# Performance work log

Measured on AMD Instinct MI355X. Metric: run time of the kernel, lower is better.

## Reference

```python
import jax, jax.numpy as jnp
import numpy as np

RADIUS = 2
B, C, D, H, W = 2, 16, 48, 128, 256
G = 3 * (2 * RADIUS + 1) ** 2  # 75 guidance channels: (2r+1)^2 spatial x 3 depth offsets


def setup_inputs() -> dict:
    key = jax.random.key(0)
    k1, k2 = jax.random.split(key)
    input1 = jax.random.normal(k1, (B, C, D, H, W), dtype=jnp.float32)  # cost volume
    input2 = jax.random.normal(k2, (B, G, H, W), dtype=jnp.float32) * 0.1  # guidance weights
    return {"input1": input1, "input2": input2}


def _lga3d(x, g, r):
    """One pass of local guided aggregation.
    x: [B,C,D,H,W] cost volume; g: [B, 3*(2r+1)^2, H, W] per-pixel weights.
    out[b,c,d,h,w] = sum_{i,j in (2r+1)^2 window, k in {d-1,d,d+1}}
                     g[b, (i*(2r+1)+j)*3+k, h, w] * x[b,c,d+k-1,h+i-r,w+j-r]
    (zero padding out of bounds; weights shared across channels)."""
    w = 2 * r + 1
    bb, cc, dd, hh, ww = x.shape
    # pad depth by 1 on each side, spatial by r on each side
    xp = jnp.pad(x, ((0, 0), (0, 0), (1, 1), (r, r), (r, r)))
    out = jnp.zeros_like(x)
    for i in range(w):          # fixed small window loop (not a data-dim loop)
        for j in range(w):
            for k in range(3):  # depth offsets -1, 0, +1
                idx = (i * w + j) * 3 + k
                patch = jax.lax.dynamic_slice(xp, (0, 0, k, i, j), (bb, cc, dd, hh, ww))
                out = out + g[:, idx][:, None, None, :, :] * patch
    return out


def reference(input1, input2):
    # '2' in LGA3D2: aggregation applied twice with the same guidance
    y = _lga3d(input1, input2, RADIUS)
    return _lga3d(y, input2, RADIUS)
```

## Files before the change

### kernel.cpp

```cpp
#include <hip/hip_runtime.h>
#include <hip/hip_bf16.h>


constexpr int RAD = 2;
constexpr int BB = 2, CC = 16, DD = 48, HH = 128, WW = 256;
constexpr int GG = 75;
constexpr int PLANE = HH * WW;

constexpr int WPT = 4;
constexpr int DPG = 4;
constexpr int NWV = 4;
constexpr int DCHUNK = 16;
constexpr int NCH = DD / DCHUNK;
constexpr int SROWS = DCHUNK + 2;
constexpr int ROWB = 528;
constexpr size_t GPB_UINTS = (size_t)BB * 5 * 9 * PLANE;

using uint = unsigned int;
typedef __attribute__((ext_vector_type(2))) _Float16 half2v;

__device__ __forceinline__ uint pkrtz(float a, float b) {
  return __builtin_bit_cast(uint, __builtin_amdgcn_cvt_pkrtz(a, b));
}
__device__ __forceinline__ float fdot2(uint a, uint b, float c) {
#if __has_builtin(__builtin_amdgcn_fdot2)
  return __builtin_amdgcn_fdot2(__builtin_bit_cast(half2v, a),
                                __builtin_bit_cast(half2v, b), c, false);
#else
  half2v av = __builtin_bit_cast(half2v, a), bv = __builtin_bit_cast(half2v, b);
  return c + (float)av.x * (float)bv.x + (float)av.y * (float)bv.y;
#endif
}
__device__ __forceinline__ uint alignp(uint a, uint b) {
  return __builtin_amdgcn_alignbit(a, b, 16);
}
__device__ __forceinline__ unsigned short f2h(float v) {
  return __builtin_bit_cast(unsigned short, (_Float16)v);
}
__device__ __forceinline__ uint getq(const uint4& v, int q) {
  return q == 0 ? v.x : q == 1 ? v.y : q == 2 ? v.z : v.w;
}

__global__ __launch_bounds__(256) void cvt_f32_f16(const float* __restrict__ x,
                                                   unsigned short* __restrict__ xh,
                                                   int n4) {
  const int stride = gridDim.x * blockDim.x;
  for (int i = blockIdx.x * blockDim.x + threadIdx.x; i < n4; i += stride) {
    const float4 v = *reinterpret_cast<const float4*>(x + (size_t)i * 4);
    uint2 u; u.x = pkrtz(v.x, v.y); u.y = pkrtz(v.z, v.w);
    *reinterpret_cast<uint2*>(xh + (size_t)i * 4) = u;
  }
}

__global__ __launch_bounds__(256) void gpack(const float* __restrict__ g,
                                             uint* __restrict__ gbuf) {
  const int n4 = (int)(GPB_UINTS / 4);
  const int stride = gridDim.x * blockDim.x;
  for (int it = blockIdx.x * blockDim.x + threadIdx.x; it < n4; it += stride) {
    const int w4 = (it % (PLANE / 4)) * 4;
    const int rest = it / (PLANE / 4);
    const int p = rest % 9;
    const int bi = rest / 9;
    const int i = bi % 5, b = bi / 5;
    const int k = p / 3, jp = p % 3;
    const int chA = (i * 5 + 2 * jp) * 3 + k;
    const float* gb = g + (size_t)b * GG * PLANE;
    const float4 a = *reinterpret_cast<const float4*>(gb + (size_t)chA * PLANE + w4);
    float4 bq = make_float4(0.f, 0.f, 0.f, 0.f);
    if (jp < 2)
      bq = *reinterpret_cast<const float4*>(gb + (size_t)(chA + 3) * PLANE + w4);
    uint4 u;
    u.x = pkrtz(a.x, bq.x); u.y = pkrtz(a.y, bq.y);
    u.z = pkrtz(a.z, bq.z); u.w = pkrtz(a.w, bq.w);
    *reinterpret_cast<uint4*>(gbuf + (size_t)it * 4) = u;
  }
}

template <typename OT, bool PACKED>
__global__ __launch_bounds__(256) void lga_pass(const unsigned short* __restrict__ x,
                                                const float* __restrict__ g,
                                                const uint* __restrict__ gpk,
                                                OT* __restrict__ out) {
  __shared__ __align__(16) unsigned char xs[2][SROWS * ROWB];

  constexpr int NWG = BB * CC * NCH * HH;
  const int bx = blockIdx.x;
  const int lid = (bx & 7) * (NWG >> 3) + (bx >> 3);
  const int dch = lid % NCH;
  const int h   = (lid / NCH) % HH;
  const int c   = (lid / (NCH * HH)) % CC;
  const int b   =  lid / (NCH * HH * CC);

  const int tid = threadIdx.x;
  const int lane = tid & 63;
  const int dg = tid >> 6;
  const int w0 = lane * WPT;
  const int d0 = dch * DCHUNK + dg * DPG;

  const unsigned short* xb = x + (size_t)(b * CC + c) * DD * PLANE;
  const float* gb = g + (size_t)b * GG * PLANE;

  if (tid < 2 * SROWS) {
    const int buf = tid / SROWS, s = tid % SROWS;
    unsigned char* r = &xs[buf][s * ROWB];
    *reinterpret_cast<uint*>(r) = 0;
    *reinterpret_cast<uint*>(r + 516) = 0;
    *reinterpret_cast<uint2*>(r + 520) = make_uint2(0, 0);
  }
  constexpr int RDW = ROWB / 4;
  if (dch == 0)
    for (int idx = tid; idx < 2 * RDW; idx += 256)
      reinterpret_cast<uint*>(&xs[idx / RDW][0])[idx % RDW] = 0;
  if (dch == NCH - 1)
    for (int idx = tid; idx < 2 * RDW; idx += 256)
      reinterpret_cast<uint*>(&xs[idx / RDW][(SROWS - 1) * ROWB])[idx % RDW] = 0;

  float acc[DPG][WPT];
#pragma unroll
  for (int a = 0; a < DPG; ++a)
#pragma unroll
    for (int q = 0; q < WPT; ++q) acc[a][q] = 0.f;

  const int ilo = (h >= RAD) ? 0 : RAD - h;
  const int him = HH - 1 + RAD - h;
  const int ihi = (him < 4) ? him : 4;

  uint2 srl[5];

  auto xstage_load = [&](int i) {
    const int hr = h + i - RAD;
#pragma unroll
    for (int t = 0; t < 5; ++t) {
      const int s = dg + NWV * t;
      if (s < SROWS &&
          !(s == 0 && dch == 0) && !(s == SROWS - 1 && dch == NCH - 1)) {
        const int dd = dch * DCHUNK + s - 1;
        srl[t] = *reinterpret_cast<const uint2*>(xb + (size_t)dd * PLANE + hr * WW + w0);
      }
    }
  };
  auto xstage_write = [&](int buf) {
#pragma unroll
    for (int t = 0; t < 5; ++t) {
      const int s = dg + NWV * t;
      if (s < SROWS &&
          !(s == 0 && dch == 0) && !(s == SROWS - 1 && dch == NCH - 1)) {
        unsigned char* rp = &xs[buf][s * ROWB + 4 + 8 * lane];
        *reinterpret_cast<uint*>(rp) = srl[t].x;
        *reinterpret_cast<uint*>(rp + 4) = srl[t].y;
      }
    }
  };

  int cur = 0;
  xstage_load(ilo);
  xstage_write(0);
  __syncthreads();

  for (int ii = ilo; ii <= ihi; ++ii) {
    uint4 G[9];
    if constexpr (PACKED) {
      const uint* gp = gpk + ((size_t)(b * 5 + ii) * 9) * PLANE + h * WW + w0;
#pragma unroll
      for (int p = 0; p < 9; ++p)
        G[p] = *reinterpret_cast<const uint4*>(gp + (size_t)p * PLANE);
    } else {
#pragma unroll
      for (int k = 0; k < 3; ++k)
#pragma unroll
        for (int jp = 0; jp < 3; ++jp) {
          const int chA = (ii * 5 + 2 * jp) * 3 + k;
          const float4 a = *reinterpret_cast<const float4*>(
              gb + (size_t)chA * PLANE + h * WW + w0);
          float4 bq = make_float4(0.f, 0.f, 0.f, 0.f);
          if (jp < 2)
            bq = *reinterpret_cast<const float4*>(
                gb + (size_t)(chA + 3) * PLANE + h * WW + w0);
          uint4 u;
          u.x = pkrtz(a.x, bq.x); u.y = pkrtz(a.y, bq.y);
          u.z = pkrtz(a.z, bq.z); u.w = pkrtz(a.w, bq.w);
          G[k * 3 + jp] = u;
        }
    }

    if (ii < ihi) xstage_load(ii + 1);

    const unsigned char* wb = &xs[cur][(dg * DPG) * ROWB] + 8 * lane;
#pragma unroll
    for (int a = -1; a <= DPG; ++a) {
      const unsigned char* rp = wb + (a + 1) * ROWB;
      const uint2 e01 = *reinterpret_cast<const uint2*>(rp);
      const uint2 e23 = *reinterpret_cast<const uint2*>(rp + 8);
      const uint  e4  = *reinterpret_cast<const uint*>(rp + 16);
      uint P[9];
      P[0] = e01.x; P[2] = e01.y; P[4] = e23.x; P[6] = e23.y; P[8] = e4;
      P[1] = alignp(P[2], P[0]);
      P[3] = alignp(P[4], P[2]);
      P[5] = alignp(P[6], P[4]);
      P[7] = alignp(P[8], P[6]);
#pragma unroll
      for (int k = 0; k < 3; ++k) {
        const int ai = a + 1 - k;
        if (ai < 0 || ai >= DPG) continue;
#pragma unroll
        for (int q = 0; q < WPT; ++q) {
          float t = acc[ai][q];
          t = fdot2(getq(G[k * 3 + 0], q), P[q], t);
          t = fdot2(getq(G[k * 3 + 1], q), P[q + 2], t);
          t = fdot2(getq(G[k * 3 + 2], q), P[q + 4], t);
          acc[ai][q] = t;
        }
      }
    }
    if (ii < ihi) xstage_write(cur ^ 1);
    __syncthreads();
    cur ^= 1;
  }

  const int obase = d0 * PLANE + h * WW + w0;
  if constexpr (sizeof(OT) == 4) {
    float* ob = (float*)out + (size_t)(b * CC + c) * DD * PLANE;
#pragma unroll
    for (int ai = 0; ai < DPG; ++ai) {
      float4 t; t.x = acc[ai][0]; t.y = acc[ai][1]; t.z = acc[ai][2]; t.w = acc[ai][3];
      *reinterpret_cast<float4*>(ob + obase + ai * PLANE) = t;
    }
  } else {
    unsigned short* ob = (unsigned short*)out + (size_t)(b * CC + c) * DD * PLANE;
#pragma unroll
    for (int ai = 0; ai < DPG; ++ai) {
      ushort4 t; t.x = f2h(acc[ai][0]); t.y = f2h(acc[ai][1]);
      t.z = f2h(acc[ai][2]); t.w = f2h(acc[ai][3]);
      *reinterpret_cast<ushort4*>(ob + obase + ai * PLANE) = t;
    }
  }
}

extern "C" void kernel_launch(void* const* d_in, const int* in_sizes, int n_in,
                              void* d_out, int out_size, void* d_ws, size_t ws_size,
                              hipStream_t stream) {
  const float* x = (const float*)d_in[0];
  const float* g = (const float*)d_in[1];
  float* out = (float*)d_out;

  const size_t elems = (size_t)BB * CC * DD * HH * WW;
  unsigned short* xh = (unsigned short*)d_out;
  unsigned short* y  = (unsigned short*)d_ws;

  cvt_f32_f16<<<2048, 256, 0, stream>>>(x, xh, (int)(elems / 4));

  const dim3 grid(BB * CC * NCH * HH);
  const dim3 block(64 * NWV);

  const size_t need = elems * 2 + GPB_UINTS * 4;
  if (ws_size >= need) {
    uint* gbuf = (uint*)((char*)d_ws + elems * 2);
    gpack<<<1440, 256, 0, stream>>>(g, gbuf);
    lga_pass<unsigned short, true><<<grid, block, 0, stream>>>(xh, g, gbuf, y);
    lga_pass<float, true><<<grid, block, 0, stream>>>(y, g, gbuf, out);
  } else {
    lga_pass<unsigned short, false><<<grid, block, 0, stream>>>(xh, g, nullptr, y);
    lga_pass<float, false><<<grid, block, 0, stream>>>(y, g, nullptr, out);
  }
}
```

Baseline: 355.6 us.

## Replace LDS double-buffered staging with direct loads and lane-shuffle halos

Removes the shared-memory double buffer, with its zero-initialisation and block-wide barriers. Each wavefront now loads its own depth rows (including the d-1 and d+1 halos) straight from global memory and gets the horizontal neighbours from adjacent lanes through ds_bpermute. This drops LDS writes and __syncthreads, but each wave now rereads the halo depth rows that were shared across waves before, and global load latency is no longer overlapped by explicit prefetch.

```diff
diff --git a/kernel.cpp b/kernel.cpp
--- a/kernel.cpp
+++ b/kernel.cpp
@@ -12,8 +12,6 @@
 constexpr int NWV = 4;
 constexpr int DCHUNK = 16;
 constexpr int NCH = DD / DCHUNK;
-constexpr int SROWS = DCHUNK + 2;
-constexpr int ROWB = 528;
 constexpr size_t GPB_UINTS = (size_t)BB * 5 * 9 * PLANE;
 
 using uint = unsigned int;
@@ -81,8 +79,6 @@
                                                 const float* __restrict__ g,
                                                 const uint* __restrict__ gpk,
                                                 OT* __restrict__ out) {
-  __shared__ __align__(16) unsigned char xs[2][SROWS * ROWB];
-
   constexpr int NWG = BB * CC * NCH * HH;
   const int bx = blockIdx.x;
   const int lid = (bx & 7) * (NWG >> 3) + (bx >> 3);
@@ -100,20 +96,10 @@
   const unsigned short* xb = x + (size_t)(b * CC + c) * DD * PLANE;
   const float* gb = g + (size_t)b * GG * PLANE;
 
-  if (tid < 2 * SROWS) {
-    const int buf = tid / SROWS, s = tid % SROWS;
-    unsigned char* r = &xs[buf][s * ROWB];
-    *reinterpret_cast<uint*>(r) = 0;
-    *reinterpret_cast<uint*>(r + 516) = 0;
-    *reinterpret_cast<uint2*>(r + 520) = make_uint2(0, 0);
-  }
-  constexpr int RDW = ROWB / 4;
-  if (dch == 0)
-    for (int idx = tid; idx < 2 * RDW; idx += 256)
-      reinterpret_cast<uint*>(&xs[idx / RDW][0])[idx % RDW] = 0;
-  if (dch == NCH - 1)
-    for (int idx = tid; idx < 2 * RDW; idx += 256)
-      reinterpret_cast<uint*>(&xs[idx / RDW][(SROWS - 1) * ROWB])[idx % RDW] = 0;
+  const int lm1 = ((lane - 1) & 63) * 4;
+  const int lp1 = ((lane + 1) & 63) * 4;
+  const bool l0 = (lane == 0);
+  const bool l63 = (lane == 63);
 
   float acc[DPG][WPT];
 #pragma unroll
@@ -125,39 +111,9 @@
   const int him = HH - 1 + RAD - h;
   const int ihi = (him < 4) ? him : 4;
 
-  uint2 srl[5];
-
-  auto xstage_load = [&](int i) {
-    const int hr = h + i - RAD;
-#pragma unroll
-    for (int t = 0; t < 5; ++t) {
-      const int s = dg + NWV * t;
-      if (s < SROWS &&
-          !(s == 0 && dch == 0) && !(s == SROWS - 1 && dch == NCH - 1)) {
-        const int dd = dch * DCHUNK + s - 1;
-        srl[t] = *reinterpret_cast<const uint2*>(xb + (size_t)dd * PLANE + hr * WW + w0);
-      }
-    }
-  };
-  auto xstage_write = [&](int buf) {
-#pragma unroll
-    for (int t = 0; t < 5; ++t) {
-      const int s = dg + NWV * t;
-      if (s < SROWS &&
-          !(s == 0 && dch == 0) && !(s == SROWS - 1 && dch == NCH - 1)) {
-        unsigned char* rp = &xs[buf][s * ROWB + 4 + 8 * lane];
-        *reinterpret_cast<uint*>(rp) = srl[t].x;
-        *reinterpret_cast<uint*>(rp + 4) = srl[t].y;
-      }
-    }
-  };
-
-  int cur = 0;
-  xstage_load(ilo);
-  xstage_write(0);
-  __syncthreads();
-
   for (int ii = ilo; ii <= ihi; ++ii) {
+    const int hr = h + ii - RAD;
+
     uint4 G[9];
     if constexpr (PACKED) {
       const uint* gp = gpk + ((size_t)(b * 5 + ii) * 9) * PLANE + h * WW + w0;
@@ -183,21 +139,30 @@
         }
     }
 
-    if (ii < ihi) xstage_load(ii + 1);
-
-    const unsigned char* wb = &xs[cur][(dg * DPG) * ROWB] + 8 * lane;
 #pragma unroll
     for (int a = -1; a <= DPG; ++a) {
-      const unsigned char* rp = wb + (a + 1) * ROWB;
-      const uint2 e01 = *reinterpret_cast<const uint2*>(rp);
-      const uint2 e23 = *reinterpret_cast<const uint2*>(rp + 8);
-      const uint  e4  = *reinterpret_cast<const uint*>(rp + 16);
+      bool dok = true;
+      if (a == -1)  dok = (d0 > 0);
+      if (a == DPG) dok = (d0 + DPG < DD);
+
+      uint2 own = make_uint2(0u, 0u);
+      if (dok)
+        own = *reinterpret_cast<const uint2*>(
+            xb + (size_t)(d0 + a) * PLANE + hr * WW + w0);
+
+      const uint lft = __builtin_amdgcn_ds_bpermute(lm1, (int)own.y);
+      const uint rg0 = __builtin_amdgcn_ds_bpermute(lp1, (int)own.x);
+      const uint rg1 = __builtin_amdgcn_ds_bpermute(lp1, (int)own.y);
       uint P[9];
-      P[0] = e01.x; P[2] = e01.y; P[4] = e23.x; P[6] = e23.y; P[8] = e4;
+      P[0] = l0 ? 0u : lft;
+      P[2] = own.x; P[4] = own.y;
+      P[6] = l63 ? 0u : rg0;
+      P[8] = l63 ? 0u : rg1;
       P[1] = alignp(P[2], P[0]);
       P[3] = alignp(P[4], P[2]);
       P[5] = alignp(P[6], P[4]);
       P[7] = alignp(P[8], P[6]);
+
 #pragma unroll
       for (int k = 0; k < 3; ++k) {
         const int ai = a + 1 - k;
@@ -212,9 +177,6 @@
         }
       }
     }
-    if (ii < ihi) xstage_write(cur ^ 1);
-    __syncthreads();
-    cur ^= 1;
   }
 
   const int obase = d0 * PLANE + h * WW + w0;
```

Result: no change. 355.3 us (-0.1%).
